# Kernel optimization log

Hardware: AMD Instinct MI355X
Metric: run time of the kernel (lower is better)

Reference implementation:

```python
import jax, jax.numpy as jnp
import numpy as np

BS, S, WIDTH, MODES = 2, 512, 64, 16
P = S * (S - 1) // 2
IU, JU = np.triu_indices(S, 1)  # upper-triangle (i<j) index constants
COLL_COEF = 0.9  # training=True path


def spectral_conv(x, w):
    # x: (bs, c_in, n), w: (c_in, c_out, modes, 2)
    n = x.shape[-1]
    xf = jnp.fft.rfft(x, axis=2, norm='ortho')  # (bs, c_in, n//2+1) complex
    wm = w[..., 0] + 1j * w[..., 1]
    out_m = jnp.einsum('bix,iox->box', xf[:, :, :MODES], wm)
    pad = jnp.zeros((x.shape[0], w.shape[1], n // 2 + 1 - MODES), dtype=out_m.dtype)
    return jnp.fft.irfft(jnp.concatenate([out_m, pad], axis=2), n=n, axis=2, norm='ortho')


def dsmc(x, a, rvec):
    # x, a: (bs, c, n); rvec: (bs, c, P) unit vectors along c.  dt=1, v = a*dt.
    bs, c, n = x.shape
    v = a
    x_r = jnp.linalg.norm(x[:, :, :, None] - x[:, :, None, :], axis=1)  # (bs, n, n)
    v_r = jnp.linalg.norm(v[:, :, :, None] - v[:, :, None, :], axis=1)
    v_cm = (v[:, :, :, None] + v[:, :, None, :]) * 0.5  # (bs, c, n, n)
    x_cm = (x[:, :, :, None] + x[:, :, None, :]) * 0.5
    u_x = jnp.exp(-x_r)
    v_r_max = jnp.max(v_r, axis=(1, 2), keepdims=True)  # (bs,1,1)
    mask = v_r / v_r_max * u_x
    cm = mask > (1.0 - COLL_COEF)  # collision mask (bs, n, n)
    # antisymmetric projection of v_r upper triangle onto random unit vectors
    proj = v_r[:, IU, JU][:, None, :] * rvec  # (bs, c, P)
    vrl = (jnp.zeros((bs, c, n, n), x.dtype)
           .at[:, :, IU, JU].set(proj)
           .at[:, :, JU, IU].set(-proj))
    delta_v = v_cm + vrl - v[:, :, :, None]
    cmf = cm.astype(x.dtype)
    v_new = v + jnp.sum(delta_v * cmf[:, None], axis=2)  # sum over partners i
    cmf = cmf + jnp.eye(n, dtype=x.dtype)[None]  # add self
    x_new = jnp.sum(x_cm * cmf[:, None], axis=2) / jnp.sum(cmf, axis=2)[:, None, :]
    x_new = x_new + v_new  # x = x + v*dt
    return x_new, v_new


def setup_inputs() -> dict:
    key = jax.random.key(0)
    ks = jax.random.split(key, 12)
    x = jax.random.normal(ks[0], (BS, S, 2), jnp.float32)
    v = jax.random.normal(ks[1], (BS, WIDTH, S), jnp.float32)
    vecs = jax.random.normal(ks[2], (4, BS, WIDTH, P), jnp.float32)
    vecs = vecs / jnp.linalg.norm(vecs, axis=2, keepdims=True)  # unit vectors over chnl
    fc0_w = jax.random.normal(ks[3], (2, WIDTH), jnp.float32) * 0.5
    fc0_b = jax.random.normal(ks[4], (WIDTH,), jnp.float32) * 0.1
    scale = 1.0 / (WIDTH * WIDTH)
    spec_w = jax.random.uniform(ks[5], (4, WIDTH, WIDTH, MODES, 2), jnp.float32) * scale
    conv_w = jax.random.normal(ks[6], (4, WIDTH, WIDTH), jnp.float32) * (WIDTH ** -0.5)
    conv_b = jax.random.normal(ks[7], (4, WIDTH), jnp.float32) * 0.05
    fc1_w = jax.random.normal(ks[8], (WIDTH, 128), jnp.float32) * (WIDTH ** -0.5)
    fc1_b = jnp.zeros((128,), jnp.float32)
    fc2_w = jax.random.normal(ks[9], (128, 1), jnp.float32) * (128 ** -0.5)
    fc2_b = jnp.zeros((1,), jnp.float32)
    return {"x": x, "v": v, "vecs": vecs, "fc0_w": fc0_w, "fc0_b": fc0_b,
            "spec_w": spec_w, "conv_w": conv_w, "conv_b": conv_b,
            "fc1_w": fc1_w, "fc1_b": fc1_b, "fc2_w": fc2_w, "fc2_b": fc2_b}


def reference(x, v, vecs, fc0_w, fc0_b, spec_w, conv_w, conv_b, fc1_w, fc1_b, fc2_w, fc2_b):
    # NOTE: v is overwritten by a*dt inside KINET_DSMC2 in the original; kept for signature fidelity.
    h = x @ fc0_w + fc0_b          # (bs, s, width)
    h = jnp.transpose(h, (0, 2, 1))  # (bs, width, s)
    for i in range(4):
        a = spectral_conv(h, spec_w[i])
        p = jnp.einsum('oi,bin->bon', conv_w[i], h) + conv_b[i][None, :, None]
        h, vv = dsmc(p, a, vecs[i])
        if i < 3:
            h = jax.nn.relu(h)
    h = jnp.transpose(h, (0, 2, 1))  # (bs, s, width)
    h = jax.nn.relu(h @ fc1_w + fc1_b)
    return h @ fc2_w + fc2_b  # (bs, s, 1)
```

## Files before the change

kernel.cpp:

```cpp
#include <hip/hip_runtime.h>
#include <math.h>

#define S 512
#define W 64
#define MODES 16
#define PAIRS 130816
#define INV_SQRT_N 0.04419417382415922f
#define TWO_PI_OVER_N 0.012271846303085130f

__global__ __launch_bounds__(256) void k_fc0(const float* __restrict__ x,
                                             const float* __restrict__ w,
                                             const float* __restrict__ bias,
                                             float* __restrict__ h) {
    int b = blockIdx.x >> 6, c = blockIdx.x & 63;
    int tid = threadIdx.x;
    float w0 = w[c], w1 = w[64 + c], bb = bias[c];
    for (int t = tid; t < S; t += 256) {
        float x0 = x[(b * S + t) * 2];
        float x1 = x[(b * S + t) * 2 + 1];
        h[(b * W + c) * S + t] = x0 * w0 + x1 * w1 + bb;
    }
}

__global__ __launch_bounds__(256) void k_fft(const float* __restrict__ h,
                                             float* __restrict__ Xf) {
    int b = blockIdx.x >> 6, ch = blockIdx.x & 63;
    int tid = threadIdx.x;
    const float* hp = h + (b * W + ch) * S;
    float v0 = hp[tid], v1 = hp[tid + 256];
    float re[MODES], im[MODES];
#pragma unroll
    for (int m = 0; m < MODES; ++m) {
        float sn, cs;
        sincosf(TWO_PI_OVER_N * (float)(m * tid), &sn, &cs);
        float a = (m & 1) ? (v0 - v1) : (v0 + v1);
        re[m] = a * cs;
        im[m] = -a * sn;
    }
    __shared__ float part[4][32];
    int lane = tid & 63, wv = tid >> 6;
#pragma unroll
    for (int m = 0; m < MODES; ++m) {
        float r = re[m], ii = im[m];
        for (int off = 32; off; off >>= 1) {
            r += __shfl_down(r, off);
            ii += __shfl_down(ii, off);
        }
        if (lane == 0) { part[wv][2 * m] = r; part[wv][2 * m + 1] = ii; }
    }
    __syncthreads();
    if (tid < 32) {
        float s = part[0][tid] + part[1][tid] + part[2][tid] + part[3][tid];
        Xf[(b * W + ch) * 32 + tid] = s * INV_SQRT_N;
    }
}

__global__ __launch_bounds__(256) void k_mix(const float* __restrict__ Xf,
                                             const float* __restrict__ specw,
                                             float* __restrict__ Y, int l) {
    int b = blockIdx.x >> 6, o = blockIdx.x & 63;
    int tid = threadIdx.x, m = tid & 15, ip = tid >> 4;
    __shared__ float Xs[2048];
    for (int idx = tid; idx < 2048; idx += 256) Xs[idx] = Xf[b * 2048 + idx];
    __syncthreads();
    float ar = 0.f, ai = 0.f;
#pragma unroll
    for (int q = 0; q < 4; ++q) {
        int i = ip * 4 + q;
        const float* wp = specw + (size_t)(((l * W + i) * W + o) * MODES + m) * 2;
        float wr = wp[0], wi = wp[1];
        float xr = Xs[i * 32 + 2 * m], xi = Xs[i * 32 + 2 * m + 1];
        ar += xr * wr - xi * wi;
        ai += xr * wi + xi * wr;
    }
    __shared__ float redr[16][17], redi[16][17];
    redr[ip][m] = ar; redi[ip][m] = ai;
    __syncthreads();
    if (tid < 16) {
        float sr = 0.f, si = 0.f;
        for (int p = 0; p < 16; ++p) { sr += redr[p][tid]; si += redi[p][tid]; }
        Y[(b * W + o) * 32 + 2 * tid] = sr;
        Y[(b * W + o) * 32 + 2 * tid + 1] = si;
    }
}

__global__ __launch_bounds__(256) void k_irfft(const float* __restrict__ Y,
                                               float* __restrict__ aT) {
    int blk = blockIdx.x;
    int b = blk >> 4, t0 = (blk & 15) * 32;
    int tid = threadIdx.x;
    int o = tid & 63, tg = tid >> 6;
    __shared__ float Ys[2048];
    for (int idx = tid; idx < 2048; idx += 256) Ys[idx] = Y[b * 2048 + idx];
    __syncthreads();
    float yr[MODES], yi[MODES];
#pragma unroll
    for (int m = 0; m < MODES; ++m) {
        yr[m] = Ys[o * 32 + 2 * m];
        yi[m] = Ys[o * 32 + 2 * m + 1];
    }
    float cc[MODES], ss[MODES], cd[MODES], sd[MODES];
#pragma unroll
    for (int m = 1; m < MODES; ++m) {
        sincosf(TWO_PI_OVER_N * (float)(m * (t0 + tg)), &ss[m], &cc[m]);
        sincosf(TWO_PI_OVER_N * (float)(4 * m), &sd[m], &cd[m]);
    }
    for (int tt = 0; tt < 8; ++tt) {
        int t = t0 + tg + 4 * tt;
        float acc = yr[0];
#pragma unroll
        for (int m = 1; m < MODES; ++m) {
            acc += 2.0f * (yr[m] * cc[m] - yi[m] * ss[m]);
            float nc = cc[m] * cd[m] - ss[m] * sd[m];
            float ns = ss[m] * cd[m] + cc[m] * sd[m];
            cc[m] = nc; ss[m] = ns;
        }
        aT[(b * S + t) * W + o] = acc * INV_SQRT_N;
    }
}

__global__ __launch_bounds__(256) void k_conv(const float* __restrict__ h,
                                              const float* __restrict__ convw,
                                              const float* __restrict__ convb,
                                              float* __restrict__ pT,
                                              unsigned* __restrict__ vmax, int l) {
    int blk = blockIdx.x;
    int b = blk >> 4, t0 = (blk & 15) * 32;
    int tid = threadIdx.x;
    int o = tid & 63, tg = tid >> 6;
    if (blk == 0 && tid < 2) vmax[tid] = 0u;
    __shared__ float hs[64 * 33];
    __shared__ float wsh[64 * 65];
    for (int idx = tid; idx < 2048; idx += 256) {
        int r = idx >> 5, t = idx & 31;
        hs[r * 33 + t] = h[(b * W + r) * S + t0 + t];
    }
    for (int idx = tid; idx < 4096; idx += 256) {
        wsh[(idx >> 6) * 65 + (idx & 63)] = convw[l * 4096 + idx];
    }
    __syncthreads();
    float wreg[64];
#pragma unroll
    for (int i = 0; i < W; ++i) wreg[i] = wsh[o * 65 + i];
    float bias = convb[l * W + o];
    for (int tt = 0; tt < 8; ++tt) {
        int tl = tg * 8 + tt;
        float acc = bias;
#pragma unroll
        for (int i = 0; i < W; ++i) acc = fmaf(wreg[i], hs[i * 33 + tl], acc);
        pT[(b * S + t0 + tl) * W + o] = acc;
    }
}

__global__ __launch_bounds__(256) void k_pair(const float* __restrict__ pT,
                                              const float* __restrict__ aT,
                                              float* __restrict__ vr,
                                              float* __restrict__ uxm,
                                              unsigned* __restrict__ vmax) {
    int blk = blockIdx.x;
    int b = blk >> 8;
    int rest = blk & 255;
    int i0 = (rest & 15) * 32, j0 = (rest >> 4) * 32;
    int tid = threadIdx.x;
    int tx = tid & 15, ty = tid >> 4;
    __shared__ float Pi[64 * 33], Pj[64 * 33], Vi[64 * 33], Vj[64 * 33];
    for (int idx = tid; idx < 2048; idx += 256) {
        int k = idx >> 6, c = idx & 63;
        Pi[c * 33 + k] = pT[(b * S + i0 + k) * W + c];
        Pj[c * 33 + k] = pT[(b * S + j0 + k) * W + c];
        Vi[c * 33 + k] = aT[(b * S + i0 + k) * W + c];
        Vj[c * 33 + k] = aT[(b * S + j0 + k) * W + c];
    }
    __syncthreads();
    float ax[2][2] = {{0.f, 0.f}, {0.f, 0.f}};
    float av[2][2] = {{0.f, 0.f}, {0.f, 0.f}};
    for (int c = 0; c < W; ++c) {
        float pi0 = Pi[c * 33 + 2 * tx], pi1 = Pi[c * 33 + 2 * tx + 1];
        float pj0 = Pj[c * 33 + 2 * ty], pj1 = Pj[c * 33 + 2 * ty + 1];
        float vi0 = Vi[c * 33 + 2 * tx], vi1 = Vi[c * 33 + 2 * tx + 1];
        float vj0 = Vj[c * 33 + 2 * ty], vj1 = Vj[c * 33 + 2 * ty + 1];
        float d;
        d = pi0 - pj0; ax[0][0] = fmaf(d, d, ax[0][0]);
        d = pi1 - pj0; ax[1][0] = fmaf(d, d, ax[1][0]);
        d = pi0 - pj1; ax[0][1] = fmaf(d, d, ax[0][1]);
        d = pi1 - pj1; ax[1][1] = fmaf(d, d, ax[1][1]);
        d = vi0 - vj0; av[0][0] = fmaf(d, d, av[0][0]);
        d = vi1 - vj0; av[1][0] = fmaf(d, d, av[1][0]);
        d = vi0 - vj1; av[0][1] = fmaf(d, d, av[0][1]);
        d = vi1 - vj1; av[1][1] = fmaf(d, d, av[1][1]);
    }
    float mx = 0.f;
#pragma unroll
    for (int jj = 0; jj < 2; ++jj) {
#pragma unroll
        for (int ii = 0; ii < 2; ++ii) {
            int i = i0 + 2 * tx + ii, j = j0 + 2 * ty + jj;
            float xr = sqrtf(ax[ii][jj]);
            float vv = sqrtf(av[ii][jj]);
            vr[((size_t)b * S + j) * S + i] = vv;
            uxm[((size_t)b * S + j) * S + i] = expf(-xr);
            mx = fmaxf(mx, vv);
        }
    }
    for (int off = 32; off; off >>= 1) mx = fmaxf(mx, __shfl_xor(mx, off));
    if ((tid & 63) == 0) atomicMax(&vmax[b], __float_as_uint(mx));
}

__global__ __launch_bounds__(256) void k_dsmc2(const float* __restrict__ pT,
                                               const float* __restrict__ aT,
                                               const float* __restrict__ vr,
                                               const float* __restrict__ uxm,
                                               const unsigned* __restrict__ vmaxu,
                                               const float* __restrict__ vecs,
                                               float* __restrict__ h_std,
                                               float* __restrict__ hT,
                                               int l, int do_relu) {
    int b = blockIdx.x >> 9;
    int j = blockIdx.x & 511;
    int tid = threadIdx.x, lane = tid & 63, wv = tid >> 6;
    __shared__ float vrow[S], urow[S];
    __shared__ int idxl[S];
    __shared__ float wl[S];
    __shared__ int pl[S];
    __shared__ int wcnt[4];
    __shared__ float SVp[4][64], SXp[4][64];
    __shared__ float Tsh[64];
    const float* vrp = vr + ((size_t)b * S + j) * S;
    const float* uxp = uxm + ((size_t)b * S + j) * S;
    for (int i = tid; i < S; i += 256) { vrow[i] = vrp[i]; urow[i] = uxp[i]; }
    __syncthreads();
    float vmax = __uint_as_float(vmaxu[b]);
    int i1 = wv * 128 + lane, i2 = i1 + 64;
    bool a1 = (vrow[i1] / vmax) * urow[i1] > 0.1f;
    bool a2 = (vrow[i2] / vmax) * urow[i2] > 0.1f;
    unsigned long long m1 = __ballot(a1), m2 = __ballot(a2);
    int c1 = (int)__popcll(m1), c2 = (int)__popcll(m2);
    if (lane == 0) wcnt[wv] = c1 + c2;
    __syncthreads();
    int off = 0;
    for (int w = 0; w < wv; ++w) off += wcnt[w];
    int A = wcnt[0] + wcnt[1] + wcnt[2] + wcnt[3];
    unsigned long long bel = (1ull << lane) - 1ull;
    if (a1) {
        int pos = off + (int)__popcll(m1 & bel);
        int i = i1;
        idxl[pos] = i;
        wl[pos] = ((i < j) ? 1.0f : -1.0f) * vrow[i];
        int lo = (i < j) ? i : j, hi = (i < j) ? j : i;
        pl[pos] = lo * 511 - ((lo * (lo - 1)) >> 1) + (hi - lo - 1);
    }
    if (a2) {
        int pos = off + c1 + (int)__popcll(m2 & bel);
        int i = i2;
        idxl[pos] = i;
        wl[pos] = ((i < j) ? 1.0f : -1.0f) * vrow[i];
        int lo = (i < j) ? i : j, hi = (i < j) ? j : i;
        pl[pos] = lo * 511 - ((lo * (lo - 1)) >> 1) + (hi - lo - 1);
    }
    __syncthreads();
    float sv = 0.f, sx = 0.f;
    for (int k = wv; k < A; k += 4) {
        int i = idxl[k];
        sv += aT[((size_t)b * S + i) * W + lane];
        sx += pT[((size_t)b * S + i) * W + lane];
    }
    SVp[wv][lane] = sv;
    SXp[wv][lane] = sx;
    const float* Rb = vecs + (size_t)((l * 2 + b) * W) * PAIRS;
    for (int cc = 0; cc < 16; ++cc) {
        int c = wv * 16 + cc;
        const float* Rc = Rb + (size_t)c * PAIRS;
        float t = 0.f;
        for (int k = lane; k < A; k += 64) t += wl[k] * Rc[pl[k]];
        for (int o2 = 32; o2; o2 >>= 1) t += __shfl_down(t, o2);
        if (lane == 0) Tsh[c] = t;
    }
    __syncthreads();
    if (tid < 64) {
        int c = tid;
        float svt = SVp[0][c] + SVp[1][c] + SVp[2][c] + SVp[3][c];
        float sxt = SXp[0][c] + SXp[1][c] + SXp[2][c] + SXp[3][c];
        float vj = aT[((size_t)b * S + j) * W + c];
        float xj = pT[((size_t)b * S + j) * W + c];
        float vnew = vj + 0.5f * ((float)A * vj - svt) + Tsh[c];
        float accx = 0.5f * ((float)A * xj + sxt);
        float xnew = (xj + accx) / (float)(A + 1) + vnew;
        if (do_relu) xnew = fmaxf(xnew, 0.0f);
        hT[((size_t)b * S + j) * W + c] = xnew;
        h_std[((size_t)b * W + c) * S + j] = xnew;
    }
}

__global__ __launch_bounds__(128) void k_head(const float* __restrict__ hT,
                                              const float* __restrict__ fc1w,
                                              const float* __restrict__ fc1b,
                                              const float* __restrict__ fc2w,
                                              const float* __restrict__ fc2b,
                                              float* __restrict__ out) {
    int blk = blockIdx.x;
    int b = blk >> 9, t = blk & 511;
    int k = threadIdx.x;
    __shared__ float hsh[64];
    __shared__ float red[2];
    if (k < 64) hsh[k] = hT[(b * S + t) * W + k];
    __syncthreads();
    float acc = fc1b[k];
#pragma unroll
    for (int c = 0; c < W; ++c) acc = fmaf(hsh[c], fc1w[c * 128 + k], acc);
    acc = fmaxf(acc, 0.f);
    float p = acc * fc2w[k];
    for (int off = 32; off; off >>= 1) p += __shfl_down(p, off);
    int lane = k & 63, wv = k >> 6;
    if (lane == 0) red[wv] = p;
    __syncthreads();
    if (k == 0) out[b * S + t] = red[0] + red[1] + fc2b[0];
}

extern "C" void kernel_launch(void* const* d_in, const int* in_sizes, int n_in,
                              void* d_out, int out_size, void* d_ws, size_t ws_size,
                              hipStream_t stream) {
    const float* x = (const float*)d_in[0];
    const float* vecs = (const float*)d_in[2];
    const float* fc0w = (const float*)d_in[3];
    const float* fc0b = (const float*)d_in[4];
    const float* specw = (const float*)d_in[5];
    const float* convw = (const float*)d_in[6];
    const float* convb = (const float*)d_in[7];
    const float* fc1w = (const float*)d_in[8];
    const float* fc1b = (const float*)d_in[9];
    const float* fc2w = (const float*)d_in[10];
    const float* fc2b = (const float*)d_in[11];
    float* out = (float*)d_out;

    char* ws = (char*)d_ws;
    unsigned* vmax = (unsigned*)ws;
    float* h_std = (float*)(ws + 256);
    float* hT = h_std + 65536;
    float* aT = hT + 65536;
    float* pT = aT + 65536;
    float* Xf = pT + 65536;
    float* Yb = Xf + 4096;
    float* vrbuf = Yb + 4096;
    float* uxbuf = vrbuf + 524288;

    k_fc0<<<128, 256, 0, stream>>>(x, fc0w, fc0b, h_std);
    for (int l = 0; l < 4; ++l) {
        k_fft<<<128, 256, 0, stream>>>(h_std, Xf);
        k_mix<<<128, 256, 0, stream>>>(Xf, specw, Yb, l);
        k_irfft<<<32, 256, 0, stream>>>(Yb, aT);
        k_conv<<<32, 256, 0, stream>>>(h_std, convw, convb, pT, vmax, l);
        k_pair<<<512, 256, 0, stream>>>(pT, aT, vrbuf, uxbuf, vmax);
        k_dsmc2<<<1024, 256, 0, stream>>>(pT, aT, vrbuf, uxbuf, vmax, vecs,
                                          h_std, hT, l, (l < 3) ? 1 : 0);
    }
    k_head<<<1024, 128, 0, stream>>>(hT, fc1w, fc1b, fc2w, fc2b, out);
}
```

Measured before the change: 770.2 us.

## Split random-vector projection into coalesced row and column passes

The per-pair projection onto random vectors is split in two. For pairs with i>j, k_dsmc2 now reads a contiguous row segment of the packed triangle, skipping 64-wide chunks that have no collisions, instead of gathering scattered entries. For pairs with i<j, a new tiled kernel k_proj handles them column-wise and accumulates into a global buffer with atomics. k_pair zeroes that buffer first. This aims to replace random gathers over the large vecs array with coalesced reads, but adds an extra launch, atomics, and some reads of non-colliding entries.

```diff
diff --git a/kernel.cpp b/kernel.cpp
--- a/kernel.cpp
+++ b/kernel.cpp
@@ -156,12 +156,14 @@
                                               const float* __restrict__ aT,
                                               float* __restrict__ vr,
                                               float* __restrict__ uxm,
-                                              unsigned* __restrict__ vmax) {
+                                              unsigned* __restrict__ vmax,
+                                              float* __restrict__ Tglob) {
     int blk = blockIdx.x;
+    int tid = threadIdx.x;
+    if (blk < 256) Tglob[blk * 256 + tid] = 0.f;
     int b = blk >> 8;
     int rest = blk & 255;
     int i0 = (rest & 15) * 32, j0 = (rest >> 4) * 32;
-    int tid = threadIdx.x;
     int tx = tid & 15, ty = tid >> 4;
     __shared__ float Pi[64 * 33], Pj[64 * 33], Vi[64 * 33], Vj[64 * 33];
     for (int idx = tid; idx < 2048; idx += 256) {
@@ -206,23 +208,76 @@
     if ((tid & 63) == 0) atomicMax(&vmax[b], __float_as_uint(mx));
 }
 
+__global__ __launch_bounds__(256) void k_proj(const float* __restrict__ vr,
+                                              const float* __restrict__ uxm,
+                                              const unsigned* __restrict__ vmaxu,
+                                              const float* __restrict__ vecs,
+                                              float* __restrict__ Tglob, int l) {
+    int tile = blockIdx.x, ch = blockIdx.y, b = blockIdx.z;
+    int ti = 0, rem = tile;
+    while (rem >= 16 - ti) { rem -= 16 - ti; ++ti; }
+    int tj = ti + rem;
+    int i0 = ti * 32, j0 = tj * 32;
+    int tid = threadIdx.x;
+    __shared__ float wt[32][33];
+    __shared__ float Tjs[4][32][32];
+    for (int k = tid; k < 4096; k += 256) ((float*)Tjs)[k] = 0.f;
+    float vmax = __uint_as_float(vmaxu[b]);
+    for (int k = tid; k < 1024; k += 256) {
+        int jj = k >> 5, ii = k & 31;
+        int gi = i0 + ii, gj = j0 + jj;
+        float vv = vr[((size_t)b * S + gj) * S + gi];
+        float uu = uxm[((size_t)b * S + gj) * S + gi];
+        float w = ((gi < gj) && ((vv / vmax) * uu > 0.1f)) ? vv : 0.f;
+        wt[ii][jj] = w;
+    }
+    __syncthreads();
+    int j = tid & 31, ig = tid >> 5, wv = tid >> 6;
+    int jg = j0 + j;
+    float w4[4];
+    int base4[4];
+#pragma unroll
+    for (int is = 0; is < 4; ++is) {
+        int il = ig * 4 + is;
+        int gi = i0 + il;
+        w4[is] = wt[il][j];
+        base4[is] = gi * 511 - ((gi * (gi - 1)) >> 1) + (jg - gi - 1);
+    }
+    const float* Rb = vecs + (size_t)((l * 2 + b) * W + ch * 32) * PAIRS;
+    for (int cc = 0; cc < 32; ++cc) {
+        const float* Rc = Rb + (size_t)cc * PAIRS;
+        float part = 0.f;
+#pragma unroll
+        for (int is = 0; is < 4; ++is)
+            if (w4[is] != 0.f) part += w4[is] * Rc[base4[is]];
+        part += __shfl_xor(part, 32);
+        if ((tid & 63) < 32) Tjs[wv][cc][j] += part;
+    }
+    __syncthreads();
+    for (int k = tid; k < 1024; k += 256) {
+        int cc = k >> 5, jj = k & 31;
+        float s = Tjs[0][cc][jj] + Tjs[1][cc][jj] + Tjs[2][cc][jj] + Tjs[3][cc][jj];
+        atomicAdd(&Tglob[((size_t)b * S + j0 + jj) * W + ch * 32 + cc], s);
+    }
+}
+
 __global__ __launch_bounds__(256) void k_dsmc2(const float* __restrict__ pT,
                                                const float* __restrict__ aT,
                                                const float* __restrict__ vr,
                                                const float* __restrict__ uxm,
                                                const unsigned* __restrict__ vmaxu,
                                                const float* __restrict__ vecs,
+                                               const float* __restrict__ Tglob,
                                                float* __restrict__ h_std,
                                                float* __restrict__ hT,
                                                int l, int do_relu) {
     int b = blockIdx.x >> 9;
     int j = blockIdx.x & 511;
     int tid = threadIdx.x, lane = tid & 63, wv = tid >> 6;
-    __shared__ float vrow[S], urow[S];
+    __shared__ float vrow[S], urow[S], wact[S];
     __shared__ int idxl[S];
-    __shared__ float wl[S];
-    __shared__ int pl[S];
     __shared__ int wcnt[4];
+    __shared__ int chunkAny[8];
     __shared__ float SVp[4][64], SXp[4][64];
     __shared__ float Tsh[64];
     const float* vrp = vr + ((size_t)b * S + j) * S;
@@ -233,30 +288,22 @@
     int i1 = wv * 128 + lane, i2 = i1 + 64;
     bool a1 = (vrow[i1] / vmax) * urow[i1] > 0.1f;
     bool a2 = (vrow[i2] / vmax) * urow[i2] > 0.1f;
+    wact[i1] = a1 ? vrow[i1] : 0.f;
+    wact[i2] = a2 ? vrow[i2] : 0.f;
     unsigned long long m1 = __ballot(a1), m2 = __ballot(a2);
     int c1 = (int)__popcll(m1), c2 = (int)__popcll(m2);
-    if (lane == 0) wcnt[wv] = c1 + c2;
+    if (lane == 0) {
+        wcnt[wv] = c1 + c2;
+        chunkAny[2 * wv] = (m1 != 0ull);
+        chunkAny[2 * wv + 1] = (m2 != 0ull);
+    }
     __syncthreads();
     int off = 0;
     for (int w = 0; w < wv; ++w) off += wcnt[w];
     int A = wcnt[0] + wcnt[1] + wcnt[2] + wcnt[3];
     unsigned long long bel = (1ull << lane) - 1ull;
-    if (a1) {
-        int pos = off + (int)__popcll(m1 & bel);
-        int i = i1;
-        idxl[pos] = i;
-        wl[pos] = ((i < j) ? 1.0f : -1.0f) * vrow[i];
-        int lo = (i < j) ? i : j, hi = (i < j) ? j : i;
-        pl[pos] = lo * 511 - ((lo * (lo - 1)) >> 1) + (hi - lo - 1);
-    }
-    if (a2) {
-        int pos = off + c1 + (int)__popcll(m2 & bel);
-        int i = i2;
-        idxl[pos] = i;
-        wl[pos] = ((i < j) ? 1.0f : -1.0f) * vrow[i];
-        int lo = (i < j) ? i : j, hi = (i < j) ? j : i;
-        pl[pos] = lo * 511 - ((lo * (lo - 1)) >> 1) + (hi - lo - 1);
-    }
+    if (a1) idxl[off + (int)__popcll(m1 & bel)] = i1;
+    if (a2) idxl[off + c1 + (int)__popcll(m2 & bel)] = i2;
     __syncthreads();
     float sv = 0.f, sx = 0.f;
     for (int k = wv; k < A; k += 4) {
@@ -266,14 +313,19 @@
     }
     SVp[wv][lane] = sv;
     SXp[wv][lane] = sx;
-    const float* Rb = vecs + (size_t)((l * 2 + b) * W) * PAIRS;
+    size_t base = (size_t)j * 511 - (((size_t)j * (j - 1)) >> 1);
+    const float* Rb = vecs + (size_t)((l * 2 + b) * W) * PAIRS + base;
     for (int cc = 0; cc < 16; ++cc) {
         int c = wv * 16 + cc;
         const float* Rc = Rb + (size_t)c * PAIRS;
         float t = 0.f;
-        for (int k = lane; k < A; k += 64) t += wl[k] * Rc[pl[k]];
+        for (int ci = 0; ci < 8; ++ci) {
+            if (!chunkAny[ci]) continue;
+            int i = ci * 64 + lane;
+            if (i > j) t += wact[i] * Rc[i - j - 1];
+        }
         for (int o2 = 32; o2; o2 >>= 1) t += __shfl_down(t, o2);
-        if (lane == 0) Tsh[c] = t;
+        if (lane == 0) Tsh[c] = -t;
     }
     __syncthreads();
     if (tid < 64) {
@@ -282,7 +334,8 @@
         float sxt = SXp[0][c] + SXp[1][c] + SXp[2][c] + SXp[3][c];
         float vj = aT[((size_t)b * S + j) * W + c];
         float xj = pT[((size_t)b * S + j) * W + c];
-        float vnew = vj + 0.5f * ((float)A * vj - svt) + Tsh[c];
+        float T = Tsh[c] + Tglob[((size_t)b * S + j) * W + c];
+        float vnew = vj + 0.5f * ((float)A * vj - svt) + T;
         float accx = 0.5f * ((float)A * xj + sxt);
         float xnew = (xj + accx) / (float)(A + 1) + vnew;
         if (do_relu) xnew = fmaxf(xnew, 0.0f);
@@ -342,6 +395,7 @@
     float* Yb = Xf + 4096;
     float* vrbuf = Yb + 4096;
     float* uxbuf = vrbuf + 524288;
+    float* Tg = uxbuf + 524288;
 
     k_fc0<<<128, 256, 0, stream>>>(x, fc0w, fc0b, h_std);
     for (int l = 0; l < 4; ++l) {
@@ -349,8 +403,9 @@
         k_mix<<<128, 256, 0, stream>>>(Xf, specw, Yb, l);
         k_irfft<<<32, 256, 0, stream>>>(Yb, aT);
         k_conv<<<32, 256, 0, stream>>>(h_std, convw, convb, pT, vmax, l);
-        k_pair<<<512, 256, 0, stream>>>(pT, aT, vrbuf, uxbuf, vmax);
-        k_dsmc2<<<1024, 256, 0, stream>>>(pT, aT, vrbuf, uxbuf, vmax, vecs,
+        k_pair<<<512, 256, 0, stream>>>(pT, aT, vrbuf, uxbuf, vmax, Tg);
+        k_proj<<<dim3(136, 2, 2), 256, 0, stream>>>(vrbuf, uxbuf, vmax, vecs, Tg, l);
+        k_dsmc2<<<1024, 256, 0, stream>>>(pT, aT, vrbuf, uxbuf, vmax, vecs, Tg,
                                           h_std, hT, l, (l < 3) ? 1 : 0);
     }
     k_head<<<1024, 128, 0, stream>>>(hT, fc1w, fc1b, fc2w, fc2b, out);
```

Result: slower. 1.079 ms (+40.2%).

## Split DSMC into mask, tiled triangular projection, and finalize kernels

Applied to the files above, without the earlier changes.

Replaces the per-row DSMC kernel with three kernels. A mask kernel writes masked pair weights into an upper-triangle buffer and computes the partner sums densely. A tiled projection kernel streams the random-vector array coalesced over 64x64 triangle tiles, using each pair once for both row j and column i with atomics. A finalize kernel combines the results. The aim is to remove the scattered gathers of vecs that happen once per row and to read vecs only once. In exchange it adds two launches, atomics and extra global buffers.

```diff
diff --git a/kernel.cpp b/kernel.cpp
--- a/kernel.cpp
+++ b/kernel.cpp
@@ -206,89 +206,134 @@
     if ((tid & 63) == 0) atomicMax(&vmax[b], __float_as_uint(mx));
 }
 
-__global__ __launch_bounds__(256) void k_dsmc2(const float* __restrict__ pT,
-                                               const float* __restrict__ aT,
-                                               const float* __restrict__ vr,
-                                               const float* __restrict__ uxm,
-                                               const unsigned* __restrict__ vmaxu,
-                                               const float* __restrict__ vecs,
-                                               float* __restrict__ h_std,
-                                               float* __restrict__ hT,
-                                               int l, int do_relu) {
-    int b = blockIdx.x >> 9;
-    int j = blockIdx.x & 511;
+__global__ __launch_bounds__(256) void k_mask(const float* __restrict__ vr,
+                                              const float* __restrict__ uxm,
+                                              const unsigned* __restrict__ vmaxu,
+                                              const float* __restrict__ aT,
+                                              const float* __restrict__ pT,
+                                              float* __restrict__ wpair,
+                                              float* __restrict__ sv,
+                                              float* __restrict__ sx,
+                                              int* __restrict__ Acnt,
+                                              float* __restrict__ Tg) {
+    int b = blockIdx.x >> 9, j = blockIdx.x & 511;
     int tid = threadIdx.x, lane = tid & 63, wv = tid >> 6;
-    __shared__ float vrow[S], urow[S];
-    __shared__ int idxl[S];
-    __shared__ float wl[S];
-    __shared__ int pl[S];
-    __shared__ int wcnt[4];
-    __shared__ float SVp[4][64], SXp[4][64];
-    __shared__ float Tsh[64];
+    __shared__ float wrow[S];
+    __shared__ float SV[4][64], SX[4][64];
+    __shared__ int cnt4[4];
     const float* vrp = vr + ((size_t)b * S + j) * S;
     const float* uxp = uxm + ((size_t)b * S + j) * S;
-    for (int i = tid; i < S; i += 256) { vrow[i] = vrp[i]; urow[i] = uxp[i]; }
-    __syncthreads();
     float vmax = __uint_as_float(vmaxu[b]);
-    int i1 = wv * 128 + lane, i2 = i1 + 64;
-    bool a1 = (vrow[i1] / vmax) * urow[i1] > 0.1f;
-    bool a2 = (vrow[i2] / vmax) * urow[i2] > 0.1f;
-    unsigned long long m1 = __ballot(a1), m2 = __ballot(a2);
-    int c1 = (int)__popcll(m1), c2 = (int)__popcll(m2);
-    if (lane == 0) wcnt[wv] = c1 + c2;
-    __syncthreads();
-    int off = 0;
-    for (int w = 0; w < wv; ++w) off += wcnt[w];
-    int A = wcnt[0] + wcnt[1] + wcnt[2] + wcnt[3];
-    unsigned long long bel = (1ull << lane) - 1ull;
-    if (a1) {
-        int pos = off + (int)__popcll(m1 & bel);
-        int i = i1;
-        idxl[pos] = i;
-        wl[pos] = ((i < j) ? 1.0f : -1.0f) * vrow[i];
-        int lo = (i < j) ? i : j, hi = (i < j) ? j : i;
-        pl[pos] = lo * 511 - ((lo * (lo - 1)) >> 1) + (hi - lo - 1);
-    }
-    if (a2) {
-        int pos = off + c1 + (int)__popcll(m2 & bel);
-        int i = i2;
-        idxl[pos] = i;
-        wl[pos] = ((i < j) ? 1.0f : -1.0f) * vrow[i];
-        int lo = (i < j) ? i : j, hi = (i < j) ? j : i;
-        pl[pos] = lo * 511 - ((lo * (lo - 1)) >> 1) + (hi - lo - 1);
-    }
-    __syncthreads();
-    float sv = 0.f, sx = 0.f;
-    for (int k = wv; k < A; k += 4) {
-        int i = idxl[k];
-        sv += aT[((size_t)b * S + i) * W + lane];
-        sx += pT[((size_t)b * S + i) * W + lane];
-    }
-    SVp[wv][lane] = sv;
-    SXp[wv][lane] = sx;
-    const float* Rb = vecs + (size_t)((l * 2 + b) * W) * PAIRS;
-    for (int cc = 0; cc < 16; ++cc) {
-        int c = wv * 16 + cc;
-        const float* Rc = Rb + (size_t)c * PAIRS;
-        float t = 0.f;
-        for (int k = lane; k < A; k += 64) t += wl[k] * Rc[pl[k]];
-        for (int o2 = 32; o2; o2 >>= 1) t += __shfl_down(t, o2);
-        if (lane == 0) Tsh[c] = t;
-    }
+    int mycnt = 0;
+    for (int i = tid; i < S; i += 256) {
+        float v = vrp[i], u = uxp[i];
+        bool act = (v / vmax) * u > 0.1f;
+        wrow[i] = act ? v : 0.f;
+        mycnt += act ? 1 : 0;
+    }
+    for (int o = 32; o; o >>= 1) mycnt += __shfl_down(mycnt, o);
+    if (lane == 0) cnt4[wv] = mycnt;
+    __syncthreads();
+    int A = cnt4[0] + cnt4[1] + cnt4[2] + cnt4[3];
+    if (tid == 0) Acnt[b * S + j] = A;
+    if (tid < 64) Tg[((size_t)b * S + j) * W + tid] = 0.f;
+    size_t tri = (size_t)j * 511 - (((size_t)j * (j - 1)) >> 1);
+    for (int i = j + 1 + tid; i < S; i += 256)
+        wpair[(size_t)b * PAIRS + tri + (i - j - 1)] = wrow[i];
+    float svp = 0.f, sxp = 0.f;
+    const float* aTb = aT + (size_t)b * S * W;
+    const float* pTb = pT + (size_t)b * S * W;
+    for (int k = 0; k < 128; ++k) {
+        int i = wv * 128 + k;
+        float w01 = (wrow[i] != 0.f) ? 1.0f : 0.0f;
+        svp = fmaf(w01, aTb[i * W + lane], svp);
+        sxp = fmaf(w01, pTb[i * W + lane], sxp);
+    }
+    SV[wv][lane] = svp; SX[wv][lane] = sxp;
     __syncthreads();
     if (tid < 64) {
-        int c = tid;
-        float svt = SVp[0][c] + SVp[1][c] + SVp[2][c] + SVp[3][c];
-        float sxt = SXp[0][c] + SXp[1][c] + SXp[2][c] + SXp[3][c];
-        float vj = aT[((size_t)b * S + j) * W + c];
-        float xj = pT[((size_t)b * S + j) * W + c];
-        float vnew = vj + 0.5f * ((float)A * vj - svt) + Tsh[c];
-        float accx = 0.5f * ((float)A * xj + sxt);
-        float xnew = (xj + accx) / (float)(A + 1) + vnew;
-        if (do_relu) xnew = fmaxf(xnew, 0.0f);
-        hT[((size_t)b * S + j) * W + c] = xnew;
-        h_std[((size_t)b * W + c) * S + j] = xnew;
-    }
+        sv[((size_t)b * S + j) * W + tid] = SV[0][tid] + SV[1][tid] + SV[2][tid] + SV[3][tid];
+        sx[((size_t)b * S + j) * W + tid] = SX[0][tid] + SX[1][tid] + SX[2][tid] + SX[3][tid];
+    }
+}
+
+__global__ __launch_bounds__(256) void k_proj2(const float* __restrict__ wpair,
+                                               const float* __restrict__ vecs,
+                                               float* __restrict__ Tg, int l) {
+    int tile = blockIdx.x, cg = blockIdx.y, b = blockIdx.z;
+    int ti = 0, rem = tile;
+    while (rem >= 8 - ti) { rem -= 8 - ti; ++ti; }
+    int tj = ti + rem;
+    int i0 = ti * 64, j0 = tj * 64;
+    int tid = threadIdx.x, lane = tid & 63, wv = tid >> 6;
+    __shared__ float Tjs[4][64][9];
+    __shared__ float Tis[64][9];
+    for (int k2 = tid; k2 < 4 * 64 * 9; k2 += 256) ((float*)Tjs)[k2] = 0.f;
+    for (int k2 = tid; k2 < 64 * 9; k2 += 256) ((float*)Tis)[k2] = 0.f;
+    __syncthreads();
+    const float* wb = wpair + (size_t)b * PAIRS;
+    const float* Rb = vecs + (size_t)((l * 2 + b) * W + cg * 8) * PAIRS;
+    float accj[8] = {0.f, 0.f, 0.f, 0.f, 0.f, 0.f, 0.f, 0.f};
+    int gj = j0 + lane;
+    for (int s = 0; s < 16; ++s) {
+        int li = wv + 4 * s;
+        int gi = i0 + li;
+        int pbase = gi * 511 - ((gi * (gi - 1)) >> 1) + (j0 - gi - 1);
+        bool valid = gj > gi;
+        int idx = valid ? (pbase + lane) : 0;
+        float w = wb[idx];
+        if (!valid) w = 0.f;
+        if (__ballot(w != 0.f) == 0ull) continue;
+        float part[8];
+#pragma unroll
+        for (int cc = 0; cc < 8; ++cc) {
+            float r = Rb[(size_t)cc * PAIRS + idx];
+            float p = w * r;
+            accj[cc] += p;
+            part[cc] = p;
+        }
+#pragma unroll
+        for (int cc = 0; cc < 8; ++cc) {
+            float p = part[cc];
+            for (int o = 32; o; o >>= 1) p += __shfl_xor(p, o);
+            if (lane == 0) Tis[li][cc] = p;
+        }
+    }
+#pragma unroll
+    for (int cc = 0; cc < 8; ++cc) Tjs[wv][lane][cc] = accj[cc];
+    __syncthreads();
+    for (int k2 = tid; k2 < 512; k2 += 256) {
+        int r = k2 >> 3, cc = k2 & 7;
+        float sj = Tjs[0][r][cc] + Tjs[1][r][cc] + Tjs[2][r][cc] + Tjs[3][r][cc];
+        if (sj != 0.f)
+            atomicAdd(&Tg[((size_t)b * S + j0 + r) * W + cg * 8 + cc], sj);
+        float si = Tis[r][cc];
+        if (si != 0.f)
+            atomicAdd(&Tg[((size_t)b * S + i0 + r) * W + cg * 8 + cc], -si);
+    }
+}
+
+__global__ __launch_bounds__(256) void k_fin(const float* __restrict__ aT,
+                                             const float* __restrict__ pT,
+                                             const float* __restrict__ sv,
+                                             const float* __restrict__ sx,
+                                             const int* __restrict__ Acnt,
+                                             const float* __restrict__ Tg,
+                                             float* __restrict__ h_std,
+                                             float* __restrict__ hT,
+                                             int do_relu) {
+    int g = blockIdx.x * 4 + (threadIdx.x >> 6);
+    int b = g >> 9, j = g & 511;
+    int c = threadIdx.x & 63;
+    size_t row = ((size_t)b * S + j) * W;
+    float A = (float)Acnt[b * S + j];
+    float vj = aT[row + c], xj = pT[row + c];
+    float vnew = vj + 0.5f * (A * vj - sv[row + c]) + Tg[row + c];
+    float accx = 0.5f * (A * xj + sx[row + c]);
+    float xnew = (xj + accx) / (A + 1.0f) + vnew;
+    if (do_relu) xnew = fmaxf(xnew, 0.0f);
+    hT[row + c] = xnew;
+    h_std[((size_t)b * W + c) * S + j] = xnew;
 }
 
 __global__ __launch_bounds__(128) void k_head(const float* __restrict__ hT,
@@ -342,6 +387,11 @@
     float* Yb = Xf + 4096;
     float* vrbuf = Yb + 4096;
     float* uxbuf = vrbuf + 524288;
+    float* Tg = uxbuf + 524288;
+    float* svb = Tg + 65536;
+    float* sxb = svb + 65536;
+    int* Acnt = (int*)(sxb + 65536);
+    float* wpair = (float*)(Acnt + 1024);
 
     k_fc0<<<128, 256, 0, stream>>>(x, fc0w, fc0b, h_std);
     for (int l = 0; l < 4; ++l) {
@@ -350,8 +400,11 @@
         k_irfft<<<32, 256, 0, stream>>>(Yb, aT);
         k_conv<<<32, 256, 0, stream>>>(h_std, convw, convb, pT, vmax, l);
         k_pair<<<512, 256, 0, stream>>>(pT, aT, vrbuf, uxbuf, vmax);
-        k_dsmc2<<<1024, 256, 0, stream>>>(pT, aT, vrbuf, uxbuf, vmax, vecs,
-                                          h_std, hT, l, (l < 3) ? 1 : 0);
+        k_mask<<<1024, 256, 0, stream>>>(vrbuf, uxbuf, vmax, aT, pT,
+                                         wpair, svb, sxb, Acnt, Tg);
+        k_proj2<<<dim3(36, 8, 2), 256, 0, stream>>>(wpair, vecs, Tg, l);
+        k_fin<<<256, 256, 0, stream>>>(aT, pT, svb, sxb, Acnt, Tg,
+                                       h_std, hT, (l < 3) ? 1 : 0);
     }
     k_head<<<1024, 128, 0, stream>>>(hT, fc1w, fc1b, fc2w, fc2b, out);
 }
```

Result: no change. 767.6 us (-0.3%).
